# Optimization experiments

Measured on AMD Instinct MI355X. Metric: run time of the kernel, lower is better.

The kernel has to match this reference:

```python
import jax, jax.numpy as jnp
import numpy as np

N_SAMPLES = 128
NEAR, FAR = 0.0, 1.0
EPS = 1e-10
FAR_DIST = 1e10


def setup_inputs() -> dict:
    key = jax.random.key(0)
    k1, k2, k3, k4 = jax.random.split(key, 4)
    N = 262144
    rays_o = jax.random.normal(k1, (N, 3), dtype=jnp.float32)
    rays_d = jax.random.normal(k2, (N, 3), dtype=jnp.float32)
    rgb = jax.random.uniform(k3, (N, N_SAMPLES, 3), dtype=jnp.float32)
    sigma = jax.random.uniform(k4, (N, N_SAMPLES, 1), dtype=jnp.float32)
    return {"rays_o": rays_o, "rays_d": rays_d, "rgb": rgb, "sigma": sigma}


def reference(rays_o, rays_d, rgb, sigma):
    N = rays_o.shape[0]
    # sample_along_rays (perturb=False): evenly spaced depths in [near, far]
    t_vals = jnp.linspace(0.0, 1.0, N_SAMPLES, dtype=jnp.float32)
    z_vals = NEAR * (1.0 - t_vals) + FAR * t_vals            # [S]
    z_vals = jnp.broadcast_to(z_vals, (N, N_SAMPLES))         # [N, S]

    # volume_rendering
    dists = z_vals[..., 1:] - z_vals[..., :-1]                # [N, S-1]
    dists = jnp.concatenate(
        [dists, jnp.full_like(dists[..., :1], FAR_DIST)], axis=-1)  # [N, S]
    dists = dists * jnp.linalg.norm(rays_d, axis=-1, keepdims=True)  # [N, S]

    alpha = 1.0 - jnp.exp(-sigma[..., 0] * dists)             # [N, S]
    trans = jnp.cumprod(
        jnp.concatenate(
            [jnp.ones_like(alpha[..., :1]), 1.0 - alpha[..., :-1] + EPS],
            axis=-1),
        axis=-1)                                              # [N, S]
    weights = alpha * trans                                   # [N, S]

    rgb_map = jnp.sum(weights[..., None] * rgb, axis=-2)      # [N, 3]
    depth_map = jnp.sum(weights * z_vals, axis=-1)            # [N]
    return rgb_map, depth_map, weights, z_vals
```

## Files before the change

kernel.cpp:

```cpp
#include <hip/hip_runtime.h>

#define NS 128
#define EPSF 1e-10f
#define FAR_DIST 1e10f

__global__ __launch_bounds__(256) void volrend_kernel(
    const float* __restrict__ rays_d,
    const float* __restrict__ rgb,
    const float* __restrict__ sigma,
    float* __restrict__ rgb_map,
    float* __restrict__ depth_map,
    float* __restrict__ weights,
    float* __restrict__ z_out,
    int N)
{
    const int wave = threadIdx.x >> 6;
    const int lane = threadIdx.x & 63;
    const int ray  = blockIdx.x * 4 + wave;
    if (ray >= N) return;

    const float dx = rays_d[ray * 3 + 0];
    const float dy = rays_d[ray * 3 + 1];
    const float dz = rays_d[ray * 3 + 2];
    const float nrm = sqrtf(dx * dx + dy * dy + dz * dz);

    const int s0 = lane * 2;
    const int s1 = s0 + 1;
    const float z0 = (float)s0 / 127.0f;
    const float z1 = (float)s1 / 127.0f;
    const float d0 = ((float)(s0 + 1) / 127.0f - z0) * nrm;
    const float d1 = (s1 == 127 ? FAR_DIST : ((float)(s1 + 1) / 127.0f - z1)) * nrm;

    const size_t base = (size_t)ray * NS;
    const float2 sg = *reinterpret_cast<const float2*>(sigma + base + s0);

    const float a0 = 1.0f - expf(-sg.x * d0);
    const float a1 = 1.0f - expf(-sg.y * d1);

    const float f0 = 1.0f - a0 + EPSF;
    const float f1 = 1.0f - a1 + EPSF;

    float p = f0 * f1;
    #pragma unroll
    for (int off = 1; off < 64; off <<= 1) {
        float t = __shfl_up(p, off);
        if (lane >= off) p *= t;
    }
    const float ex = __shfl_up(p, 1);
    const float trans0 = (lane == 0) ? 1.0f : ex;
    const float trans1 = trans0 * f0;

    const float w0 = a0 * trans0;
    const float w1 = a1 * trans1;

    *reinterpret_cast<float2*>(weights + base + s0) = make_float2(w0, w1);
    *reinterpret_cast<float2*>(z_out   + base + s0) = make_float2(z0, z1);

    const float* rrow = rgb + (size_t)ray * NS * 3 + 6 * lane;
    const float2 v0 = *reinterpret_cast<const float2*>(rrow + 0);
    const float2 v1 = *reinterpret_cast<const float2*>(rrow + 2);
    const float2 v2 = *reinterpret_cast<const float2*>(rrow + 4);
    float accr = w0 * v0.x + w1 * v1.y;
    float accg = w0 * v0.y + w1 * v2.x;
    float accb = w0 * v1.x + w1 * v2.y;
    float accd = w0 * z0 + w1 * z1;

    #pragma unroll
    for (int off = 32; off >= 1; off >>= 1) {
        accr += __shfl_down(accr, off);
        accg += __shfl_down(accg, off);
        accb += __shfl_down(accb, off);
        accd += __shfl_down(accd, off);
    }
    if (lane == 0) {
        rgb_map[(size_t)ray * 3 + 0] = accr;
        rgb_map[(size_t)ray * 3 + 1] = accg;
        rgb_map[(size_t)ray * 3 + 2] = accb;
        depth_map[ray] = accd;
    }
}

extern "C" void kernel_launch(void* const* d_in, const int* in_sizes, int n_in,
                              void* d_out, int out_size, void* d_ws, size_t ws_size,
                              hipStream_t stream) {
    const float* rays_d = (const float*)d_in[1];
    const float* rgb    = (const float*)d_in[2];
    const float* sigma  = (const float*)d_in[3];
    const int N = in_sizes[0] / 3;

    float* out       = (float*)d_out;
    float* rgb_map   = out;
    float* depth_map = out + (size_t)N * 3;
    float* weights   = out + (size_t)N * 4;
    float* z_vals    = out + (size_t)N * 4 + (size_t)N * NS;

    const int blocks = (N + 3) / 4;
    volrend_kernel<<<blocks, 256, 0, stream>>>(
        rays_d, rgb, sigma, rgb_map, depth_map, weights, z_vals, N);
}
```

Before: 668.4 us.

## Process two rays per wavefront with four samples per lane and float4 accesses

Each wavefront now handles two rays, one per 32-lane half, and each lane covers four consecutive samples instead of two. Sigma, weights, z and rgb are moved with float4 instead of float2, the scan and reduction run over 32 lanes, and expf is swapped for __expf. The aim is fewer shuffle steps per ray, wider memory transactions and fewer blocks for this bandwidth-bound kernel, at the cost of more registers and slightly lower exp precision.

```diff
diff --git a/kernel.cpp b/kernel.cpp
--- a/kernel.cpp
+++ b/kernel.cpp
@@ -14,9 +14,11 @@
     float* __restrict__ z_out,
     int N)
 {
-    const int wave = threadIdx.x >> 6;
+    const int wid  = threadIdx.x >> 6;
     const int lane = threadIdx.x & 63;
-    const int ray  = blockIdx.x * 4 + wave;
+    const int half = lane >> 5;
+    const int sl   = lane & 31;
+    const int ray  = (blockIdx.x * 4 + wid) * 2 + half;
     if (ray >= N) return;
 
     const float dx = rays_d[ray * 3 + 0];
@@ -24,55 +26,64 @@
     const float dz = rays_d[ray * 3 + 2];
     const float nrm = sqrtf(dx * dx + dy * dy + dz * dz);
 
-    const int s0 = lane * 2;
-    const int s1 = s0 + 1;
-    const float z0 = (float)s0 / 127.0f;
-    const float z1 = (float)s1 / 127.0f;
-    const float d0 = ((float)(s0 + 1) / 127.0f - z0) * nrm;
-    const float d1 = (s1 == 127 ? FAR_DIST : ((float)(s1 + 1) / 127.0f - z1)) * nrm;
+    const int s = sl * 4;
+    const float c = 1.0f / 127.0f;
+    float z[4], d[4];
+    #pragma unroll
+    for (int j = 0; j < 4; ++j) {
+        z[j] = (float)(s + j) * c;
+        const float zn = (float)(s + j + 1) * c;
+        d[j] = ((s + j == 127) ? FAR_DIST : (zn - z[j])) * nrm;
+    }
 
-    const size_t base = (size_t)ray * NS;
-    const float2 sg = *reinterpret_cast<const float2*>(sigma + base + s0);
+    const size_t base = (size_t)ray * NS + s;
+    const float4 sg = *reinterpret_cast<const float4*>(sigma + base);
 
-    const float a0 = 1.0f - expf(-sg.x * d0);
-    const float a1 = 1.0f - expf(-sg.y * d1);
+    float a[4], f[4];
+    a[0] = 1.0f - __expf(-sg.x * d[0]);
+    a[1] = 1.0f - __expf(-sg.y * d[1]);
+    a[2] = 1.0f - __expf(-sg.z * d[2]);
+    a[3] = 1.0f - __expf(-sg.w * d[3]);
+    #pragma unroll
+    for (int j = 0; j < 4; ++j) f[j] = 1.0f - a[j] + EPSF;
 
-    const float f0 = 1.0f - a0 + EPSF;
-    const float f1 = 1.0f - a1 + EPSF;
+    float p = (f[0] * f[1]) * (f[2] * f[3]);
+    #pragma unroll
+    for (int off = 1; off < 32; off <<= 1) {
+        const float t = __shfl_up(p, off, 32);
+        if (sl >= off) p *= t;
+    }
+    const float ex = __shfl_up(p, 1, 32);
+    float t0 = (sl == 0) ? 1.0f : ex;
+    const float t1 = t0 * f[0];
+    const float t2 = t1 * f[1];
+    const float t3 = t2 * f[2];
 
-    float p = f0 * f1;
-    #pragma unroll
-    for (int off = 1; off < 64; off <<= 1) {
-        float t = __shfl_up(p, off);
-        if (lane >= off) p *= t;
-    }
-    const float ex = __shfl_up(p, 1);
-    const float trans0 = (lane == 0) ? 1.0f : ex;
-    const float trans1 = trans0 * f0;
+    const float w0 = a[0] * t0;
+    const float w1 = a[1] * t1;
+    const float w2 = a[2] * t2;
+    const float w3 = a[3] * t3;
 
-    const float w0 = a0 * trans0;
-    const float w1 = a1 * trans1;
+    *reinterpret_cast<float4*>(weights + base) = make_float4(w0, w1, w2, w3);
+    *reinterpret_cast<float4*>(z_out   + base) = make_float4(z[0], z[1], z[2], z[3]);
 
-    *reinterpret_cast<float2*>(weights + base + s0) = make_float2(w0, w1);
-    *reinterpret_cast<float2*>(z_out   + base + s0) = make_float2(z0, z1);
-
-    const float* rrow = rgb + (size_t)ray * NS * 3 + 6 * lane;
-    const float2 v0 = *reinterpret_cast<const float2*>(rrow + 0);
-    const float2 v1 = *reinterpret_cast<const float2*>(rrow + 2);
-    const float2 v2 = *reinterpret_cast<const float2*>(rrow + 4);
-    float accr = w0 * v0.x + w1 * v1.y;
-    float accg = w0 * v0.y + w1 * v2.x;
-    float accb = w0 * v1.x + w1 * v2.y;
-    float accd = w0 * z0 + w1 * z1;
+    const float* rrow = rgb + (size_t)ray * NS * 3 + 12 * sl;
+    const float4 u0 = *reinterpret_cast<const float4*>(rrow + 0);
+    const float4 u1 = *reinterpret_cast<const float4*>(rrow + 4);
+    const float4 u2 = *reinterpret_cast<const float4*>(rrow + 8);
+    float accr = w0 * u0.x + w1 * u0.w + w2 * u1.z + w3 * u2.y;
+    float accg = w0 * u0.y + w1 * u1.x + w2 * u1.w + w3 * u2.z;
+    float accb = w0 * u0.z + w1 * u1.y + w2 * u2.x + w3 * u2.w;
+    float accd = w0 * z[0] + w1 * z[1] + w2 * z[2] + w3 * z[3];
 
     #pragma unroll
-    for (int off = 32; off >= 1; off >>= 1) {
-        accr += __shfl_down(accr, off);
-        accg += __shfl_down(accg, off);
-        accb += __shfl_down(accb, off);
-        accd += __shfl_down(accd, off);
+    for (int off = 16; off >= 1; off >>= 1) {
+        accr += __shfl_down(accr, off, 32);
+        accg += __shfl_down(accg, off, 32);
+        accb += __shfl_down(accb, off, 32);
+        accd += __shfl_down(accd, off, 32);
     }
-    if (lane == 0) {
+    if (sl == 0) {
         rgb_map[(size_t)ray * 3 + 0] = accr;
         rgb_map[(size_t)ray * 3 + 1] = accg;
         rgb_map[(size_t)ray * 3 + 2] = accb;
@@ -94,7 +105,7 @@
     float* weights   = out + (size_t)N * 4;
     float* z_vals    = out + (size_t)N * 4 + (size_t)N * NS;
 
-    const int blocks = (N + 3) / 4;
+    const int blocks = (N + 7) / 8;
     volrend_kernel<<<blocks, 256, 0, stream>>>(
         rays_d, rgb, sigma, rgb_map, depth_map, weights, z_vals, N);
 }
```

Measured after the change: 666.5 us. No clear change (-0.3%).
